# Optimization experiments

Hardware: AMD Instinct MI355X
Metric: run time of the kernel (lower is better)

The kernel has to match this reference:

```python
import jax, jax.numpy as jnp
import numpy as np


def setup_inputs() -> dict:
    key = jax.random.key(0)
    k1, k2 = jax.random.split(key)
    B, Lq, Ls, D = 16, 2048, 2048, 512
    query = jax.random.normal(k1, (B, Lq, D), dtype=jnp.float32)
    support = jax.random.normal(k2, (B, Ls, D), dtype=jnp.float32)
    return {"query": query, "support": support}


def reference(query, support):
    # attn: [B, Lq, Ls] = softmax(query @ support^T, axis=-1)
    logits = jnp.einsum("bqd,bsd->bqs", query, support)
    attn = jax.nn.softmax(logits, axis=-1)
    # attended support: [B, Lq, D]
    attended = jnp.einsum("bqs,bsd->bqd", attn, support)
    # score: [B, Lq] = sum over D of query * attended
    score = jnp.sum(query * attended, axis=-1)
    return score
```

## Files before the change

kernel.cpp:

```cpp
#include <hip/hip_runtime.h>
#include <hip/hip_bf16.h>

#define B_  16
#define LQ  2048
#define LS  2048
#define DD  512
#define BQ  256
#define BS  256
#define BK  64
#define NSB (LS / BS)
#define NKC (DD / BK)
#define NSPLIT 4

static_assert(NKC == 8, "stage>>3 math assumes NKC==8");

typedef short bf16x8 __attribute__((ext_vector_type(8)));
typedef float f32x4  __attribute__((ext_vector_type(4)));

__device__ __forceinline__ void load_lds16(const void* g, void* l) {
  __builtin_amdgcn_global_load_lds((const __attribute__((address_space(1))) void*)g,
                                   (__attribute__((address_space(3))) void*)l,
                                   16, 0, 0);
}

__device__ __forceinline__ unsigned short f2bf(float f) {
  union { float f; unsigned int u; } v; v.f = f;
  unsigned int r = v.u + 0x7fffu + ((v.u >> 16) & 1u);
  return (unsigned short)(r >> 16);
}

__global__ __launch_bounds__(256) void cvt_kernel(const float* __restrict__ Q,
                                                  const float* __restrict__ S,
                                                  unsigned short* __restrict__ Qw,
                                                  unsigned short* __restrict__ Sw,
                                                  int nblk) {
  int blk = blockIdx.x;
  const float* src; unsigned short* dst;
  if (blk < nblk) { src = Q; dst = Qw; } else { src = S; dst = Sw; blk -= nblk; }
  int i = blk * 256 + threadIdx.x;
  float4 f = ((const float4*)src)[i];
  ushort4 u;
  u.x = f2bf(f.x); u.y = f2bf(f.y); u.z = f2bf(f.z); u.w = f2bf(f.w);
  ((ushort4*)dst)[i] = u;
}

__global__ __launch_bounds__(512, 2) void attn_kernel(const unsigned short* __restrict__ Qw,
                                                      const unsigned short* __restrict__ Sw,
                                                      float* __restrict__ out,
                                                      float* __restrict__ pm,
                                                      float* __restrict__ pse,
                                                      float* __restrict__ psel,
                                                      int nsplit) {
  __shared__ __align__(16) unsigned short sQ[2][BQ * BK];
  __shared__ __align__(16) unsigned short sS[2][BS * BK];

  const int pid = blockIdx.x + (blockIdx.y << 3) + (blockIdx.z << 7);
  const int nch = (nsplit << 7) >> 3;
  const int lid = (pid & 7) * nch + (pid >> 3);
  const int qb  = lid & 7;
  const int b   = (lid >> 3) & 15;
  const int spl = lid >> 7;

  const int tid  = threadIdx.x;
  const int w    = tid >> 6;
  const int lane = tid & 63;
  const int h    = w & 1;
  const int g    = w >> 1;
  const int col  = lane & 15;
  const int quad = lane >> 4;
  const int c7   = col & 7;

  const int q0 = qb * BQ;
  const unsigned short* Qb = Qw + (size_t)b * LQ * DD;
  const unsigned short* Sb = Sw + (size_t)b * LS * DD;

  float mst[4] = { -INFINITY, -INFINITY, -INFINITY, -INFINITY };
  float se[4]  = { 0.f, 0.f, 0.f, 0.f };
  float sel[4] = { 0.f, 0.f, 0.f, 0.f };

  f32x4 acc[8][4];
#pragma unroll
  for (int st = 0; st < 8; ++st)
#pragma unroll
    for (int qt = 0; qt < 4; ++qt)
      acc[st][qt] = (f32x4){0.f, 0.f, 0.f, 0.f};

  const int rr = lane >> 3;
  const int cc = ((lane & 7) ^ rr) * 8;

  const int sbs = spl * (NSB / nsplit);
  const int nst = (NSB / nsplit) * NKC;

  auto issue_stage = [&](int t_i, int buf) {
    const int kc = t_i & 7;
    if (w < 4) {
      const unsigned short* gp = Qb + (size_t)(q0 + w * 64 + rr) * DD + kc * BK + cc;
      unsigned short* lp = &sQ[buf][(w * 64) * BK];
#pragma unroll
      for (int i = 0; i < 8; ++i)
        load_lds16(gp + (size_t)i * 8 * DD, lp + i * 8 * BK);
    } else {
      const int sb = sbs + (t_i >> 3);
      const unsigned short* gp = Sb + (size_t)(sb * BS + (w - 4) * 64 + rr) * DD + kc * BK + cc;
      unsigned short* lp = &sS[buf][((w - 4) * 64) * BK];
#pragma unroll
      for (int i = 0; i < 8; ++i)
        load_lds16(gp + (size_t)i * 8 * DD, lp + i * 8 * BK);
    }
  };

  issue_stage(0, 0);
  int cur = 0;

#pragma unroll 1
  for (int t = 0; t < nst; ++t) {
    asm volatile("s_waitcnt lgkmcnt(0)" ::: "memory");
    __builtin_amdgcn_s_barrier();

    const int tn = t + 1;
    if (tn < nst) {
      issue_stage(tn, cur ^ 1);
      asm volatile("s_waitcnt vmcnt(8)" ::: "memory");
    } else {
      asm volatile("s_waitcnt vmcnt(0)" ::: "memory");
    }
    __builtin_amdgcn_s_barrier();
    __builtin_amdgcn_sched_barrier(0);

    const unsigned short* bq = &sQ[cur][0];
    const unsigned short* bs = &sS[cur][0];
    __builtin_amdgcn_s_setprio(1);
#pragma unroll
    for (int kk = 0; kk < 2; ++kk) {
      const int koff = ((kk * 4 + quad) ^ c7) * 8;
      bf16x8 asv[8];
#pragma unroll
      for (int st = 0; st < 8; ++st)
        asv[st] = *(const bf16x8*)&bs[(h * 128 + st * 16 + col) * BK + koff];
#pragma unroll
      for (int qt = 0; qt < 4; ++qt) {
        bf16x8 aq = *(const bf16x8*)&bq[(g * 64 + qt * 16 + col) * BK + koff];
#pragma unroll
        for (int st = 0; st < 8; ++st)
          acc[st][qt] = __builtin_amdgcn_mfma_f32_16x16x32_bf16(asv[st], aq, acc[st][qt], 0, 0, 0);
      }
    }
    __builtin_amdgcn_s_setprio(0);
    cur ^= 1;

    if ((t & (NKC - 1)) == NKC - 1) {
#pragma unroll
      for (int qt = 0; qt < 4; ++qt) {
        float lmax = mst[qt];
#pragma unroll
        for (int st = 0; st < 8; ++st)
#pragma unroll
          for (int r = 0; r < 4; ++r)
            lmax = fmaxf(lmax, acc[st][qt][r]);
        lmax = fmaxf(lmax, __shfl_xor(lmax, 16, 64));
        lmax = fmaxf(lmax, __shfl_xor(lmax, 32, 64));
        float alpha = __expf(mst[qt] - lmax);
        float pe = 0.f, pel = 0.f;
#pragma unroll
        for (int st = 0; st < 8; ++st)
#pragma unroll
          for (int r = 0; r < 4; ++r) {
            float l = acc[st][qt][r];
            float e = __expf(l - lmax);
            pe += e;
            pel = fmaf(e, l, pel);
          }
        pe  += __shfl_xor(pe, 16, 64);  pe  += __shfl_xor(pe, 32, 64);
        pel += __shfl_xor(pel, 16, 64); pel += __shfl_xor(pel, 32, 64);
        se[qt]  = fmaf(se[qt],  alpha, pe);
        sel[qt] = fmaf(sel[qt], alpha, pel);
        mst[qt] = lmax;
#pragma unroll
        for (int st = 0; st < 8; ++st)
          acc[st][qt] = (f32x4){0.f, 0.f, 0.f, 0.f};
      }
    }
  }

  __syncthreads();
  float* red = (float*)&sQ[0][0];
  if (quad == 0) {
#pragma unroll
    for (int qt = 0; qt < 4; ++qt) {
      int qq = g * 64 + qt * 16 + col;
      red[h * 256 + qq]        = mst[qt];
      red[512 + h * 256 + qq]  = se[qt];
      red[1024 + h * 256 + qq] = sel[qt];
    }
  }
  __syncthreads();
  if (h == 0 && quad == 0) {
#pragma unroll
    for (int qt = 0; qt < 4; ++qt) {
      int qq = g * 64 + qt * 16 + col;
      float m0 = red[qq],       m1 = red[256 + qq];
      float M  = fmaxf(m0, m1);
      float a0 = __expf(m0 - M), a1 = __expf(m1 - M);
      float SE  = red[512 + qq]  * a0 + red[512 + 256 + qq]  * a1;
      float SEL = red[1024 + qq] * a0 + red[1024 + 256 + qq] * a1;
      size_t qi = (size_t)b * LQ + q0 + qq;
      if (nsplit == 1) {
        out[qi] = SEL / SE;
      } else {
        pm[qi * NSPLIT + spl]   = M;
        pse[qi * NSPLIT + spl]  = SE;
        psel[qi * NSPLIT + spl] = SEL;
      }
    }
  }
}

__global__ __launch_bounds__(256) void combine_kernel(const float* __restrict__ pm,
                                                      const float* __restrict__ pse,
                                                      const float* __restrict__ psel,
                                                      float* __restrict__ out) {
  int i = blockIdx.x * blockDim.x + threadIdx.x;
  if (i >= B_ * LQ) return;
  float M = -INFINITY;
#pragma unroll
  for (int s = 0; s < NSPLIT; ++s) M = fmaxf(M, pm[i * NSPLIT + s]);
  float SE = 0.f, SEL = 0.f;
#pragma unroll
  for (int s = 0; s < NSPLIT; ++s) {
    float a = __expf(pm[i * NSPLIT + s] - M);
    SE  = fmaf(pse[i * NSPLIT + s],  a, SE);
    SEL = fmaf(psel[i * NSPLIT + s], a, SEL);
  }
  out[i] = SEL / SE;
}

__global__ __launch_bounds__(256) void fallback_kernel(const float* __restrict__ Q,
                                                       const float* __restrict__ S,
                                                       float* __restrict__ out) {
  __shared__ float qv[DD];
  __shared__ float red[256];
  const int b = blockIdx.y, qi = blockIdx.x, tid = threadIdx.x;
  const float* qrow = Q + ((size_t)b * LQ + qi) * DD;
  for (int d = tid; d < DD; d += 256) qv[d] = qrow[d];
  __syncthreads();
  const float* Sb = S + (size_t)b * LS * DD;
  float m = -INFINITY, se = 0.f, sel = 0.f;
  for (int s = tid; s < LS; s += 256) {
    const float* srow = Sb + (size_t)s * DD;
    float dot = 0.f;
    for (int d = 0; d < DD; ++d) dot = fmaf(qv[d], srow[d], dot);
    float mn = fmaxf(m, dot);
    float a = __expf(m - mn);
    float e = __expf(dot - mn);
    se  = se * a + e;
    sel = sel * a + e * dot;
    m = mn;
  }
  red[tid] = m; __syncthreads();
  for (int o = 128; o > 0; o >>= 1) { if (tid < o) red[tid] = fmaxf(red[tid], red[tid + o]); __syncthreads(); }
  float M = red[0]; __syncthreads();
  float a = __expf(m - M); se *= a; sel *= a;
  red[tid] = se; __syncthreads();
  for (int o = 128; o > 0; o >>= 1) { if (tid < o) red[tid] += red[tid + o]; __syncthreads(); }
  float SE = red[0]; __syncthreads();
  red[tid] = sel; __syncthreads();
  for (int o = 128; o > 0; o >>= 1) { if (tid < o) red[tid] += red[tid + o]; __syncthreads(); }
  float SEL = red[0];
  if (tid == 0) out[(size_t)b * LQ + qi] = SEL / SE;
}

extern "C" void kernel_launch(void* const* d_in, const int* in_sizes, int n_in,
                              void* d_out, int out_size, void* d_ws, size_t ws_size,
                              hipStream_t stream) {
  const float* Q = (const float*)d_in[0];
  const float* S = (const float*)d_in[1];
  float* out = (float*)d_out;
  const size_t nelem = (size_t)B_ * LQ * DD;
  const size_t need_base  = 2 * nelem * sizeof(unsigned short);
  const size_t part_elems = (size_t)B_ * LQ * NSPLIT;
  const size_t need_split = need_base + 3 * part_elems * sizeof(float);

  if (ws_size >= need_base) {
    unsigned short* Qw = (unsigned short*)d_ws;
    unsigned short* Sw = Qw + nelem;
    int nblk = (int)(nelem / 4 / 256);
    cvt_kernel<<<2 * nblk, 256, 0, stream>>>(Q, S, Qw, Sw, nblk);
    if (ws_size >= need_split) {
      float* pm   = (float*)(Sw + nelem);
      float* pse  = pm + part_elems;
      float* psel = pse + part_elems;
      attn_kernel<<<dim3(LQ / BQ, B_, NSPLIT), 512, 0, stream>>>(Qw, Sw, out, pm, pse, psel, NSPLIT);
      combine_kernel<<<(B_ * LQ + 255) / 256, 256, 0, stream>>>(pm, pse, psel, out);
    } else {
      attn_kernel<<<dim3(LQ / BQ, B_, 1), 512, 0, stream>>>(Qw, Sw, out, nullptr, nullptr, nullptr, 1);
    }
  } else {
    fallback_kernel<<<dim3(LQ, B_), 256, 0, stream>>>(Q, S, out);
  }
}
```

Baseline: 221.3 us.

## Switch to 32x32x16 MFMA and interleave LDS prefetch with k-substeps

Replaces the 16x16x32 bf16 MFMA tiling with 32x32x16 MFMAs: each wave now holds 4x2 accumulator tiles of 16 floats, which cuts the number of LDS operand reads per FLOP and the cross-lane shuffles in the softmax reduction. The main loop is also restructured into four k-substeps, each with its own barriers. The next stage's global-to-LDS loads are issued at the first substep, and the wait for them happens only at the last substep. This adds more barriers per tile and changes the synchronisation pattern, which risks stalls or hazards on the double buffer.

```diff
diff --git a/kernel.cpp b/kernel.cpp
--- a/kernel.cpp
+++ b/kernel.cpp
@@ -16,6 +16,7 @@
 
 typedef short bf16x8 __attribute__((ext_vector_type(8)));
 typedef float f32x4  __attribute__((ext_vector_type(4)));
+typedef float f32x16 __attribute__((ext_vector_type(16)));
 
 __device__ __forceinline__ void load_lds16(const void* g, void* l) {
   __builtin_amdgcn_global_load_lds((const __attribute__((address_space(1))) void*)g,
@@ -66,24 +67,24 @@
   const int lane = tid & 63;
   const int h    = w & 1;
   const int g    = w >> 1;
-  const int col  = lane & 15;
-  const int quad = lane >> 4;
-  const int c7   = col & 7;
+  const int r5   = lane & 31;
+  const int hi   = lane >> 5;
+  const int l7   = lane & 7;
 
   const int q0 = qb * BQ;
   const unsigned short* Qb = Qw + (size_t)b * LQ * DD;
   const unsigned short* Sb = Sw + (size_t)b * LS * DD;
 
-  float mst[4] = { -INFINITY, -INFINITY, -INFINITY, -INFINITY };
-  float se[4]  = { 0.f, 0.f, 0.f, 0.f };
-  float sel[4] = { 0.f, 0.f, 0.f, 0.f };
-
-  f32x4 acc[8][4];
-#pragma unroll
-  for (int st = 0; st < 8; ++st)
-#pragma unroll
-    for (int qt = 0; qt < 4; ++qt)
-      acc[st][qt] = (f32x4){0.f, 0.f, 0.f, 0.f};
+  float mst[2] = { -INFINITY, -INFINITY };
+  float se[2]  = { 0.f, 0.f };
+  float sel[2] = { 0.f, 0.f };
+
+  f32x16 acc[4][2];
+#pragma unroll
+  for (int st = 0; st < 4; ++st)
+#pragma unroll
+    for (int qt = 0; qt < 2; ++qt)
+      acc[st][qt] = (f32x16){0.f,0.f,0.f,0.f,0.f,0.f,0.f,0.f,0.f,0.f,0.f,0.f,0.f,0.f,0.f,0.f};
 
   const int rr = lane >> 3;
   const int cc = ((lane & 7) ^ rr) * 8;
@@ -110,94 +111,92 @@
   };
 
   issue_stage(0, 0);
+  asm volatile("s_waitcnt vmcnt(0)" ::: "memory");
+  __builtin_amdgcn_s_barrier();
   int cur = 0;
 
 #pragma unroll 1
   for (int t = 0; t < nst; ++t) {
-    asm volatile("s_waitcnt lgkmcnt(0)" ::: "memory");
-    __builtin_amdgcn_s_barrier();
-
     const int tn = t + 1;
-    if (tn < nst) {
-      issue_stage(tn, cur ^ 1);
-      asm volatile("s_waitcnt vmcnt(8)" ::: "memory");
-    } else {
-      asm volatile("s_waitcnt vmcnt(0)" ::: "memory");
-    }
-    __builtin_amdgcn_s_barrier();
-    __builtin_amdgcn_sched_barrier(0);
-
     const unsigned short* bq = &sQ[cur][0];
     const unsigned short* bs = &sS[cur][0];
-    __builtin_amdgcn_s_setprio(1);
-#pragma unroll
-    for (int kk = 0; kk < 2; ++kk) {
-      const int koff = ((kk * 4 + quad) ^ c7) * 8;
-      bf16x8 asv[8];
-#pragma unroll
-      for (int st = 0; st < 8; ++st)
-        asv[st] = *(const bf16x8*)&bs[(h * 128 + st * 16 + col) * BK + koff];
-#pragma unroll
-      for (int qt = 0; qt < 4; ++qt) {
-        bf16x8 aq = *(const bf16x8*)&bq[(g * 64 + qt * 16 + col) * BK + koff];
-#pragma unroll
-        for (int st = 0; st < 8; ++st)
-          acc[st][qt] = __builtin_amdgcn_mfma_f32_16x16x32_bf16(asv[st], aq, acc[st][qt], 0, 0, 0);
-      }
-    }
-    __builtin_amdgcn_s_setprio(0);
+
+#pragma unroll
+    for (int ks = 0; ks < 4; ++ks) {
+      if (ks == 0 && tn < nst) issue_stage(tn, cur ^ 1);
+      const int koff = (((ks << 1) | hi) ^ l7) * 8;
+      bf16x8 asv[4], aq[2];
+#pragma unroll
+      for (int st = 0; st < 4; ++st)
+        asv[st] = *(const bf16x8*)&bs[(h * 128 + st * 32 + r5) * BK + koff];
+#pragma unroll
+      for (int qt = 0; qt < 2; ++qt)
+        aq[qt] = *(const bf16x8*)&bq[(g * 64 + qt * 32 + r5) * BK + koff];
+      __builtin_amdgcn_s_barrier();
+      asm volatile("s_waitcnt lgkmcnt(0)" ::: "memory");
+      __builtin_amdgcn_sched_barrier(0);
+      __builtin_amdgcn_s_setprio(1);
+#pragma unroll
+      for (int qt = 0; qt < 2; ++qt)
+#pragma unroll
+        for (int st = 0; st < 4; ++st)
+          acc[st][qt] = __builtin_amdgcn_mfma_f32_32x32x16_bf16(asv[st], aq[qt], acc[st][qt], 0, 0, 0);
+      __builtin_amdgcn_s_setprio(0);
+      if (ks == 3)
+        asm volatile("s_waitcnt vmcnt(0)" ::: "memory");
+      __builtin_amdgcn_s_barrier();
+    }
     cur ^= 1;
 
     if ((t & (NKC - 1)) == NKC - 1) {
 #pragma unroll
-      for (int qt = 0; qt < 4; ++qt) {
+      for (int qt = 0; qt < 2; ++qt) {
         float lmax = mst[qt];
 #pragma unroll
-        for (int st = 0; st < 8; ++st)
-#pragma unroll
-          for (int r = 0; r < 4; ++r)
+        for (int st = 0; st < 4; ++st)
+#pragma unroll
+          for (int r = 0; r < 16; ++r)
             lmax = fmaxf(lmax, acc[st][qt][r]);
-        lmax = fmaxf(lmax, __shfl_xor(lmax, 16, 64));
         lmax = fmaxf(lmax, __shfl_xor(lmax, 32, 64));
         float alpha = __expf(mst[qt] - lmax);
         float pe = 0.f, pel = 0.f;
 #pragma unroll
-        for (int st = 0; st < 8; ++st)
-#pragma unroll
-          for (int r = 0; r < 4; ++r) {
+        for (int st = 0; st < 4; ++st)
+#pragma unroll
+          for (int r = 0; r < 16; ++r) {
             float l = acc[st][qt][r];
             float e = __expf(l - lmax);
             pe += e;
             pel = fmaf(e, l, pel);
           }
-        pe  += __shfl_xor(pe, 16, 64);  pe  += __shfl_xor(pe, 32, 64);
-        pel += __shfl_xor(pel, 16, 64); pel += __shfl_xor(pel, 32, 64);
+        pe  += __shfl_xor(pe, 32, 64);
+        pel += __shfl_xor(pel, 32, 64);
         se[qt]  = fmaf(se[qt],  alpha, pe);
         sel[qt] = fmaf(sel[qt], alpha, pel);
         mst[qt] = lmax;
 #pragma unroll
-        for (int st = 0; st < 8; ++st)
-          acc[st][qt] = (f32x4){0.f, 0.f, 0.f, 0.f};
+        for (int st = 0; st < 4; ++st)
+          acc[st][qt] = (f32x16){0.f,0.f,0.f,0.f,0.f,0.f,0.f,0.f,0.f,0.f,0.f,0.f,0.f,0.f,0.f,0.f};
       }
     }
   }
 
   __syncthreads();
   float* red = (float*)&sQ[0][0];
-  if (quad == 0) {
-#pragma unroll
-    for (int qt = 0; qt < 4; ++qt) {
-      int qq = g * 64 + qt * 16 + col;
+  if (hi == 0) {
+#pragma unroll
+    for (int qt = 0; qt < 2; ++qt) {
+      int qq = g * 64 + qt * 32 + r5;
       red[h * 256 + qq]        = mst[qt];
       red[512 + h * 256 + qq]  = se[qt];
       red[1024 + h * 256 + qq] = sel[qt];
     }
   }
   __syncthreads();
-  if (h == 0 && quad == 0) {
-#pragma unroll
-    for (int qt = 0; qt < 4; ++qt) {
-      int qq = g * 64 + qt * 16 + col;
+  if (h == 0 && hi == 0) {
+#pragma unroll
+    for (int qt = 0; qt < 2; ++qt) {
+      int qq = g * 64 + qt * 32 + r5;
       float m0 = red[qq],       m1 = red[256 + qq];
       float M  = fmaxf(m0, m1);
       float a0 = __expf(m0 - M), a1 = __expf(m1 - M);
```

New measurement: 234.9 us. 1.06x slower.
